# Optimization experiments

Measured on AMD Instinct MI355X. Metric: run time of the kernel, lower is better.

The kernel has to match this reference:

```python
import jax, jax.numpy as jnp
import numpy as np

H_SPLITS = [2, 3, 3]          # crpe_window {3:2, 5:3, 7:3}
K_SIZES = [3, 5, 7]
NUM_HEADS = 8
EPS = 1e-6


def dwconv(x, w, b, k):
    # x: (B,C,H,W), w: (C,1,k,k) depthwise, 'same' padding
    y = jax.lax.conv_general_dilated(
        x, w, (1, 1), [(k // 2, k // 2)] * 2,
        feature_group_count=x.shape[1],
        dimension_numbers=('NCHW', 'OIHW', 'NCHW'))
    return y + b[None, :, None, None]


def layernorm(x, g, b):
    m = jnp.mean(x, -1, keepdims=True)
    v = jnp.var(x, -1, keepdims=True)
    return (x - m) * jax.lax.rsqrt(v + EPS) * g + b


def conv_rel_pos_enc(q, v, ws, bs, H, W):
    # ConvRelPosEnc (MPViT style, no cls token): q * depthwise_conv(v)
    B, h, N, Ch = q.shape
    v_img = v.transpose(0, 1, 3, 2).reshape(B, h * Ch, H, W)  # B (h Ch) H W
    splits = np.cumsum([hs * Ch for hs in H_SPLITS])[:-1]
    parts = jnp.split(v_img, splits, axis=1)
    conv_v = jnp.concatenate(
        [dwconv(p, w, b, k) for p, w, b, k in zip(parts, ws, bs, K_SIZES)], axis=1)
    conv_v = conv_v.reshape(B, h, Ch, N).transpose(0, 1, 3, 2)
    return q * conv_v


def setup_inputs() -> dict:
    key = jax.random.key(0)
    B, H, W, C, nd, r, mr = 8, 64, 64, 320, 4, 2, 4
    h = NUM_HEADS
    N = H * W
    Ch = C // h
    hid = C // r
    ks = jax.random.split(key, 16)
    s = 0.02
    return {
        'x': jax.random.normal(ks[0], (B, N, C), jnp.float32),
        'domain_label': jax.nn.one_hot(jax.random.randint(ks[1], (B,), 0, nd), nd, dtype=jnp.float32),
        'cpe_w': jax.random.normal(ks[2], (C, 1, 3, 3), jnp.float32) * s,
        'cpe_b': jnp.zeros((C,), jnp.float32),
        'ln1_g': jnp.ones((C,), jnp.float32), 'ln1_b': jnp.zeros((C,), jnp.float32),
        'qkv_w': jax.random.normal(ks[3], (3 * C, C), jnp.float32) * s,
        'qkv_b': jnp.zeros((3 * C,), jnp.float32),
        'crpe_w3': jax.random.normal(ks[4], (2 * Ch, 1, 3, 3), jnp.float32) * s,
        'crpe_b3': jnp.zeros((2 * Ch,), jnp.float32),
        'crpe_w5': jax.random.normal(ks[5], (3 * Ch, 1, 5, 5), jnp.float32) * s,
        'crpe_b5': jnp.zeros((3 * Ch,), jnp.float32),
        'crpe_w7': jax.random.normal(ks[6], (3 * Ch, 1, 7, 7), jnp.float32) * s,
        'crpe_b7': jnp.zeros((3 * Ch,), jnp.float32),
        'dom_w1': jax.random.normal(ks[7], (hid, nd), jnp.float32) * s,
        'dom_b1': jnp.zeros((hid,), jnp.float32),
        'dom_w2': jax.random.normal(ks[8], (C, hid), jnp.float32) * s,
        'dom_b2': jnp.zeros((C,), jnp.float32),
        'proj_w': jax.random.normal(ks[9], (C, C), jnp.float32) * s,
        'proj_b': jnp.zeros((C,), jnp.float32),
        'ln2_g': jnp.ones((C,), jnp.float32), 'ln2_b': jnp.zeros((C,), jnp.float32),
        'mlp_w1': jax.random.normal(ks[10], (mr * C, C), jnp.float32) * s,
        'mlp_b1': jnp.zeros((mr * C,), jnp.float32),
        'mlp_w2': jax.random.normal(ks[11], (C, mr * C), jnp.float32) * s,
        'mlp_b2': jnp.zeros((C,), jnp.float32),
        'H': H, 'W': W,
    }


def reference(x, domain_label, cpe_w, cpe_b, ln1_g, ln1_b, qkv_w, qkv_b,
              crpe_w3, crpe_b3, crpe_w5, crpe_b5, crpe_w7, crpe_b7,
              dom_w1, dom_b1, dom_w2, dom_b2, proj_w, proj_b,
              ln2_g, ln2_b, mlp_w1, mlp_b1, mlp_w2, mlp_b2, H, W):
    B, N, C = x.shape
    h = NUM_HEADS
    Ch = C // h
    scale = Ch ** -0.5
    # ConvPosEnc: depthwise 3x3 conv + residual
    img = x.transpose(0, 2, 1).reshape(B, C, H, W)
    x = (dwconv(img, cpe_w, cpe_b, 3) + img).reshape(B, C, N).transpose(0, 2, 1)
    # FactorAtt_ConvRelPosEnc_Sup
    cur = layernorm(x, ln1_g, ln1_b)
    qkv = (cur @ qkv_w.T + qkv_b).reshape(B, N, 3, h, Ch).transpose(2, 0, 3, 1, 4)
    q, k, v = qkv[0], qkv[1], qkv[2]          # (B,h,N,Ch) each
    k_sm = jax.nn.softmax(k, axis=2)          # softmax over tokens
    kv = jnp.einsum('bhnk,bhnv->bhkv', k_sm, v)   # (B,h,Ch,Ch)
    fa = jnp.einsum('bhnk,bhkv->bhnv', q, kv)
    fa = scale * fa + conv_rel_pos_enc(
        q, v, (crpe_w3, crpe_w5, crpe_w7), (crpe_b3, crpe_b5, crpe_b7), H, W)
    # domain gate: MLP(one_hot) -> softmax over heads, broadcast over tokens
    d = jax.nn.relu(domain_label @ dom_w1.T + dom_b1) @ dom_w2.T + dom_b2  # (B,C)
    d = jax.nn.softmax(d.reshape(B, h, 1, Ch), axis=1)
    att = (d * fa).transpose(0, 2, 1, 3).reshape(B, N, C)
    x = x + (att @ proj_w.T + proj_b)
    # MLP (GELU, ratio 4)
    cur = layernorm(x, ln2_g, ln2_b)
    cur = jax.nn.gelu(cur @ mlp_w1.T + mlp_b1, approximate=False) @ mlp_w2.T + mlp_b2
    return x + cur
```

## Files before the change

kernel.cpp:

```cpp
#include <hip/hip_runtime.h>
#include <hip/hip_bf16.h>
#include <math.h>
#include <type_traits>

#define B_    8
#define Nn    4096
#define Cc    320
#define QS    1024
#define ATT_SCALE 0.15811388300841897f

typedef __attribute__((ext_vector_type(8))) short s8v;
typedef __attribute__((ext_vector_type(4))) float f4v;

__device__ __forceinline__ float bf2f(short u) {
    return __uint_as_float(((unsigned int)(unsigned short)u) << 16);
}
__device__ __forceinline__ short f2bf(float f) {
    return (short)__bfloat16_as_ushort(__float2bfloat16(f));
}
__device__ __forceinline__ float gelu_fast(float v) {
    float u = v * (0.7978845608f + 0.0356774081f * v * v);
    float e = __expf(2.f * u);
    float t = 1.f - 2.f / (e + 1.f);
    return 0.5f * v * (1.f + t);
}

typedef const __attribute__((address_space(1))) unsigned int* gp1_t;
typedef __attribute__((address_space(3))) unsigned int* lp3_t;
__device__ __forceinline__ void gload16(const void* g, void* l) {
    __builtin_amdgcn_global_load_lds((gp1_t)g, (lp3_t)l, 16, 0, 0);
}

__global__ void cvt_all(const float* __restrict__ s0, const float* __restrict__ s1,
                        const float* __restrict__ s2, const float* __restrict__ s3,
                        __hip_bfloat16* __restrict__ d) {
    int i = blockIdx.x * 256 + threadIdx.x;
    if (i >= 1351680) return;
    const float* s; int j, rows, K;
    if (i < 327680)      { s = s0; j = i;          rows = 960;  K = 320; }
    else if (i < 450560) { s = s1; j = i - 327680; rows = 320;  K = 320; }
    else if (i < 860160) { s = s2; j = i - 450560; rows = 1280; K = 320; }
    else                 { s = s3; j = i - 860160; rows = 320;  K = 1280; }
    float v = (j / K < rows) ? s[j] : 0.f;
    d[i] = __float2bfloat16(v);
}

template<typename T>
__global__ void ln_kernel(const T* __restrict__ x, const float* __restrict__ g,
                          const float* __restrict__ bt, __hip_bfloat16* __restrict__ out) {
    int bn = blockIdx.x;
    int lane = threadIdx.x;
    const T* row = x + (size_t)bn * Cc;
    float v[5];
    float s = 0.f, s2 = 0.f;
    #pragma unroll
    for (int i = 0; i < 5; ++i) {
        if constexpr (std::is_same<T, float>::value) v[i] = row[lane + 64 * i];
        else v[i] = bf2f(((const short*)row)[lane + 64 * i]);
        s += v[i];
        s2 += v[i] * v[i];
    }
    #pragma unroll
    for (int off = 32; off > 0; off >>= 1) {
        s  += __shfl_down(s, off);
        s2 += __shfl_down(s2, off);
    }
    s  = __shfl(s, 0);
    s2 = __shfl(s2, 0);
    float mean = s * (1.f / 320.f);
    float var  = s2 * (1.f / 320.f) - mean * mean;
    float rstd = rsqrtf(var + 1e-6f);
    __hip_bfloat16* orow = out + (size_t)bn * Cc;
    #pragma unroll
    for (int i = 0; i < 5; ++i) {
        int c = lane + 64 * i;
        orow[c] = __float2bfloat16((v[i] - mean) * rstd * g[c] + bt[c]);
    }
}

template<int ACT, int RES, int WF32, int WBF16, int KT>
__global__ __launch_bounds__(512) void gemm_mfma(
        const __hip_bfloat16* __restrict__ A, const __hip_bfloat16* __restrict__ W,
        const float* __restrict__ bias, const void* __restrict__ resv,
        float* __restrict__ outf, __hip_bfloat16* __restrict__ outb,
        int NS, int Nreal, int gy) {
    constexpr int NSTEP = KT / 32;
    __shared__ __align__(16) short As[2][256 * 32];
    __shared__ __align__(16) short Bs[2][128 * 32];
    int bid = blockIdx.x;
    int grp8 = gy << 3;
    int grp = bid / grp8, rem = bid % grp8;
    int m0 = ((grp << 3) + (rem & 7)) << 8;
    int n0 = (rem >> 3) << 7;
    int tid = threadIdx.x;
    int w = tid >> 6, lane = tid & 63;
    int wr = w >> 1, wc = w & 1;
    int lrow = lane & 15, lk = lane >> 4;
    f4v acc[4][4];
    #pragma unroll
    for (int i = 0; i < 4; ++i)
        #pragma unroll
        for (int j = 0; j < 4; ++j) acc[i][j] = (f4v){0.f, 0.f, 0.f, 0.f};

    int ua0 = (w << 6) + lane;
    auto STAGE = [&](int buf, int k0) {
        #pragma unroll
        for (int i = 0; i < 2; ++i) {
            int u = ua0 + i * 512;
            int row = u >> 2, slot = u & 3;
            int sk = (slot ^ (row & 3)) << 3;
            gload16(&A[(size_t)(m0 + row) * KT + k0 + sk], &As[buf][i * 4096 + w * 512]);
        }
        {
            int u = ua0;
            int row = u >> 2, slot = u & 3;
            int sk = (slot ^ (row & 3)) << 3;
            gload16(&W[(size_t)(n0 + row) * KT + k0 + sk], &Bs[buf][w * 512]);
        }
    };

    STAGE(0, 0);
    #pragma unroll
    for (int step = 0; step < NSTEP; ++step) {
        int buf = step & 1;
        if (step + 1 < NSTEP) {
            STAGE(buf ^ 1, (step + 1) * 32);
            asm volatile("s_waitcnt vmcnt(3)" ::: "memory");
        } else {
            asm volatile("s_waitcnt vmcnt(0)" ::: "memory");
        }
        __builtin_amdgcn_sched_barrier(0);
        __builtin_amdgcn_s_barrier();
        s8v af[4], bf[4];
        #pragma unroll
        for (int mi = 0; mi < 4; ++mi) {
            int row = wr * 64 + mi * 16 + lrow;
            af[mi] = *reinterpret_cast<const s8v*>(&As[buf][row * 32 + ((lk ^ (row & 3)) << 3)]);
        }
        #pragma unroll
        for (int ni = 0; ni < 4; ++ni) {
            int row = wc * 64 + ni * 16 + lrow;
            bf[ni] = *reinterpret_cast<const s8v*>(&Bs[buf][row * 32 + ((lk ^ (row & 3)) << 3)]);
        }
        #pragma unroll
        for (int mi = 0; mi < 4; ++mi)
            #pragma unroll
            for (int ni = 0; ni < 4; ++ni)
                acc[mi][ni] = __builtin_amdgcn_mfma_f32_16x16x32_bf16(bf[ni], af[mi], acc[mi][ni], 0, 0, 0);
        __builtin_amdgcn_s_barrier();
    }
    #pragma unroll
    for (int mi = 0; mi < 4; ++mi) {
        int m = m0 + wr * 64 + mi * 16 + lrow;
        #pragma unroll
        for (int ni = 0; ni < 4; ++ni) {
            int n = n0 + wc * 64 + ni * 16 + (lk << 2);
            if (n >= Nreal) continue;
            f4v v4 = acc[mi][ni];
            float4 bv = *reinterpret_cast<const float4*>(&bias[n]);
            v4[0] += bv.x; v4[1] += bv.y; v4[2] += bv.z; v4[3] += bv.w;
            if (RES == 1) {
                const float* res = (const float*)resv;
                float4 rv = *reinterpret_cast<const float4*>(&res[(size_t)m * NS + n]);
                v4[0] += rv.x; v4[1] += rv.y; v4[2] += rv.z; v4[3] += rv.w;
            } else if (RES == 2) {
                const short* res = (const short*)resv;
                short4 rv = *reinterpret_cast<const short4*>(&res[(size_t)m * NS + n]);
                v4[0] += bf2f(rv.x); v4[1] += bf2f(rv.y);
                v4[2] += bf2f(rv.z); v4[3] += bf2f(rv.w);
            }
            if (ACT == 1) {
                #pragma unroll
                for (int r = 0; r < 4; ++r) v4[r] = gelu_fast(v4[r]);
            }
            if (WF32)
                *reinterpret_cast<float4*>(&outf[(size_t)m * NS + n]) =
                    make_float4(v4[0], v4[1], v4[2], v4[3]);
            if (WBF16) {
                ushort4 u;
                u.x = (unsigned short)f2bf(v4[0]);
                u.y = (unsigned short)f2bf(v4[1]);
                u.z = (unsigned short)f2bf(v4[2]);
                u.w = (unsigned short)f2bf(v4[3]);
                *reinterpret_cast<ushort4*>(&outb[(size_t)m * NS + n]) = u;
            }
        }
    }
}

template<int ACT, int RES, int WF32, int WBF16, int KT, int LN>
__global__ __launch_bounds__(512) void gemm_fulln(
        const __hip_bfloat16* __restrict__ A, const __hip_bfloat16* __restrict__ W,
        const float* __restrict__ bias, const void* __restrict__ resv,
        float* __restrict__ outf, __hip_bfloat16* __restrict__ outb, int NS,
        const float* __restrict__ lng, const float* __restrict__ lnb,
        __hip_bfloat16* __restrict__ lnout) {
    __shared__ __align__(16) short As[64 * 64];
    __shared__ __align__(16) short Ws[320 * 64];
    int tid = threadIdx.x;
    int m0 = blockIdx.x << 6;
    int w = tid >> 6, lane = tid & 63;
    int wr = w >> 2, wc = w & 3;
    int lrow = lane & 15, lk = lane >> 4;
    f4v acc[2][5];
    #pragma unroll
    for (int i = 0; i < 2; ++i)
        #pragma unroll
        for (int j = 0; j < 5; ++j) acc[i][j] = (f4v){0.f, 0.f, 0.f, 0.f};

    int srow = tid >> 3;
    int slot = tid & 7;

    #pragma unroll
    for (int k0 = 0; k0 < KT; k0 += 64) {
        __syncthreads();
        {
            int sk = (slot ^ (srow & 7)) << 3;
            gload16(&A[(size_t)(m0 + srow) * KT + k0 + sk], &As[w * 512]);
        }
        #pragma unroll
        for (int i = 0; i < 5; ++i) {
            int row = i * 64 + srow;
            int sk = (slot ^ (row & 7)) << 3;
            gload16(&W[(size_t)row * KT + k0 + sk], &Ws[i * 4096 + w * 512]);
        }
        __syncthreads();
        #pragma unroll
        for (int ks = 0; ks < 2; ++ks) {
            s8v af[2], bf[5];
            #pragma unroll
            for (int mi = 0; mi < 2; ++mi) {
                int row = wr * 32 + mi * 16 + lrow;
                int s = (ks * 4 + lk) ^ (row & 7);
                af[mi] = *reinterpret_cast<const s8v*>(&As[row * 64 + s * 8]);
            }
            #pragma unroll
            for (int ni = 0; ni < 5; ++ni) {
                int row = wc * 80 + ni * 16 + lrow;
                int s = (ks * 4 + lk) ^ (row & 7);
                bf[ni] = *reinterpret_cast<const s8v*>(&Ws[row * 64 + s * 8]);
            }
            #pragma unroll
            for (int mi = 0; mi < 2; ++mi)
                #pragma unroll
                for (int ni = 0; ni < 5; ++ni)
                    acc[mi][ni] = __builtin_amdgcn_mfma_f32_16x16x32_bf16(bf[ni], af[mi], acc[mi][ni], 0, 0, 0);
        }
    }
    float psum[2] = {0.f, 0.f}, psq[2] = {0.f, 0.f};
    #pragma unroll
    for (int mi = 0; mi < 2; ++mi) {
        int rl = wr * 32 + mi * 16 + lrow;
        int m = m0 + rl;
        #pragma unroll
        for (int ni = 0; ni < 5; ++ni) {
            int n = wc * 80 + ni * 16 + (lk << 2);
            f4v v4 = acc[mi][ni];
            float4 bv = *reinterpret_cast<const float4*>(&bias[n]);
            v4[0] += bv.x; v4[1] += bv.y; v4[2] += bv.z; v4[3] += bv.w;
            if (RES == 1) {
                const float* res = (const float*)resv;
                float4 rv = *reinterpret_cast<const float4*>(&res[(size_t)m * NS + n]);
                v4[0] += rv.x; v4[1] += rv.y; v4[2] += rv.z; v4[3] += rv.w;
            } else if (RES == 2) {
                const short* res = (const short*)resv;
                short4 rv = *reinterpret_cast<const short4*>(&res[(size_t)m * NS + n]);
                v4[0] += bf2f(rv.x); v4[1] += bf2f(rv.y);
                v4[2] += bf2f(rv.z); v4[3] += bf2f(rv.w);
            }
            if (ACT == 1) {
                #pragma unroll
                for (int r = 0; r < 4; ++r) v4[r] = gelu_fast(v4[r]);
            }
            if (WF32)
                *reinterpret_cast<float4*>(&outf[(size_t)m * NS + n]) =
                    make_float4(v4[0], v4[1], v4[2], v4[3]);
            if (WBF16) {
                ushort4 u;
                u.x = (unsigned short)f2bf(v4[0]);
                u.y = (unsigned short)f2bf(v4[1]);
                u.z = (unsigned short)f2bf(v4[2]);
                u.w = (unsigned short)f2bf(v4[3]);
                *reinterpret_cast<ushort4*>(&outb[(size_t)m * NS + n]) = u;
            }
            if (LN) {
                acc[mi][ni] = v4;
                psum[mi] += v4[0] + v4[1] + v4[2] + v4[3];
                psq[mi]  += v4[0]*v4[0] + v4[1]*v4[1] + v4[2]*v4[2] + v4[3]*v4[3];
            }
        }
    }
    if (LN) {
        __syncthreads();
        float* red = (float*)As;
        #pragma unroll
        for (int mi = 0; mi < 2; ++mi) {
            int rl = wr * 32 + mi * 16 + lrow;
            red[(rl * 16 + wc * 4 + lk) * 2]     = psum[mi];
            red[(rl * 16 + wc * 4 + lk) * 2 + 1] = psq[mi];
        }
        __syncthreads();
        float* st = (float*)Ws;
        if (tid < 64) {
            float s = 0.f, q = 0.f;
            #pragma unroll
            for (int p = 0; p < 16; ++p) {
                s += red[(tid * 16 + p) * 2];
                q += red[(tid * 16 + p) * 2 + 1];
            }
            float mean = s * (1.f / 320.f);
            float var  = q * (1.f / 320.f) - mean * mean;
            st[tid * 2]     = mean;
            st[tid * 2 + 1] = rsqrtf(var + 1e-6f);
        }
        __syncthreads();
        #pragma unroll
        for (int mi = 0; mi < 2; ++mi) {
            int rl = wr * 32 + mi * 16 + lrow;
            int m = m0 + rl;
            float mean = st[rl * 2], rstd = st[rl * 2 + 1];
            #pragma unroll
            for (int ni = 0; ni < 5; ++ni) {
                int n = wc * 80 + ni * 16 + (lk << 2);
                float4 g4 = *reinterpret_cast<const float4*>(&lng[n]);
                float4 b4 = *reinterpret_cast<const float4*>(&lnb[n]);
                f4v v4 = acc[mi][ni];
                ushort4 u;
                u.x = (unsigned short)f2bf((v4[0] - mean) * rstd * g4.x + b4.x);
                u.y = (unsigned short)f2bf((v4[1] - mean) * rstd * g4.y + b4.y);
                u.z = (unsigned short)f2bf((v4[2] - mean) * rstd * g4.z + b4.z);
                u.w = (unsigned short)f2bf((v4[3] - mean) * rstd * g4.w + b4.w);
                *reinterpret_cast<ushort4*>(&lnout[(size_t)m * Cc + n]) = u;
            }
        }
    }
}

__global__ __launch_bounds__(256) void cpe_tile(
        const float* __restrict__ src, const float* __restrict__ wts,
        const float* __restrict__ bias, __hip_bfloat16* __restrict__ outb) {
    constexpr int P = 1, S = 18;
    __shared__ float vt[S * S * 8];
    __shared__ float ws_[8 * 9];
    int blk = blockIdx.x;
    int tile = blk & 15;
    int g  = (blk >> 4) % 40;
    int b  = (blk >> 4) / 40;
    int ty0 = (tile >> 2) << 4;
    int tx0 = (tile & 3) << 4;
    int c0 = g * 8;
    int tid = threadIdx.x;
    for (int e = tid; e < 72; e += 256) ws_[e] = wts[c0 * 9 + e];
    const float* sb = src + (size_t)b * Nn * Cc + c0;
    for (int e = tid; e < S * S; e += 256) {
        int hy = e / S, hx = e % S;
        int gy = ty0 - P + hy, gx = tx0 - P + hx;
        float px8[8];
        #pragma unroll
        for (int j = 0; j < 8; ++j) px8[j] = 0.f;
        if ((unsigned)gy < 64u && (unsigned)gx < 64u) {
            const float* p = &sb[(size_t)((gy << 6) + gx) * Cc];
            float4 lo = reinterpret_cast<const float4*>(p)[0];
            float4 hi = reinterpret_cast<const float4*>(p)[1];
            px8[0] = lo.x; px8[1] = lo.y; px8[2] = lo.z; px8[3] = lo.w;
            px8[4] = hi.x; px8[5] = hi.y; px8[6] = hi.z; px8[7] = hi.w;
        }
        #pragma unroll
        for (int j = 0; j < 8; ++j) vt[e * 8 + j] = px8[j];
    }
    __syncthreads();
    int cl  = tid & 7;
    int px  = (tid >> 3) & 15;
    int pyh = tid >> 7;
    int c = c0 + cl;
    float acc[8];
    float bval = bias[c];
    #pragma unroll
    for (int j = 0; j < 8; ++j) acc[j] = bval;
    #pragma unroll
    for (int dx = 0; dx < 3; ++dx) {
        float col[10];
        #pragma unroll
        for (int i = 0; i < 10; ++i)
            col[i] = vt[((pyh * 8 + i) * S + (px + dx)) * 8 + cl];
        #pragma unroll
        for (int j = 0; j < 8; ++j)
            #pragma unroll
            for (int dy = 0; dy < 3; ++dy)
                acc[j] += col[j + dy] * ws_[cl * 9 + dy * 3 + dx];
    }
    #pragma unroll
    for (int j = 0; j < 8; ++j) {
        int n = ((ty0 + pyh * 8 + j) << 6) + tx0 + px;
        size_t bn = (size_t)b * Nn + n;
        float ctr = vt[((pyh * 8 + j + P) * S + (px + P)) * 8 + cl];
        outb[bn * Cc + c] = __float2bfloat16(acc[j] + ctr);
    }
}

template<int KSZ>
__device__ __forceinline__ void crpe_body(
        float* vt, float* ws_, int tile, int b, int c0,
        const short* __restrict__ qkv, const float* __restrict__ wts,
        const float* __restrict__ bias,
        const short* __restrict__ fa0, const float* __restrict__ dg,
        short* __restrict__ outb) {
    constexpr int P = KSZ / 2;
    constexpr int S = 16 + 2 * P;
    int ty0 = (tile >> 2) << 4;
    int tx0 = (tile & 3) << 4;
    int tid = threadIdx.x;
    for (int e = tid; e < 8 * KSZ * KSZ; e += 256) ws_[e] = wts[e];
    const short* sb = qkv + (size_t)b * Nn * QS + 640 + c0;
    for (int e = tid; e < S * S; e += 256) {
        int hy = e / S, hx = e % S;
        int gy = ty0 - P + hy, gx = tx0 - P + hx;
        float px8[8];
        #pragma unroll
        for (int j = 0; j < 8; ++j) px8[j] = 0.f;
        if ((unsigned)gy < 64u && (unsigned)gx < 64u) {
            s8v v8 = *reinterpret_cast<const s8v*>(&sb[(size_t)((gy << 6) + gx) * QS]);
            #pragma unroll
            for (int j = 0; j < 8; ++j) px8[j] = bf2f(v8[j]);
        }
        #pragma unroll
        for (int j = 0; j < 8; ++j) vt[e * 8 + j] = px8[j];
    }
    __syncthreads();
    int cl  = tid & 7;
    int px  = (tid >> 3) & 15;
    int pyh = tid >> 7;
    int c = c0 + cl;
    float acc[8];
    float bval = bias[cl];
    #pragma unroll
    for (int j = 0; j < 8; ++j) acc[j] = bval;
    #pragma unroll
    for (int dx = 0; dx < KSZ; ++dx) {
        float col[8 + KSZ - 1];
        #pragma unroll
        for (int i = 0; i < 8 + KSZ - 1; ++i)
            col[i] = vt[((pyh * 8 + i) * S + (px + dx)) * 8 + cl];
        #pragma unroll
        for (int j = 0; j < 8; ++j)
            #pragma unroll
            for (int dy = 0; dy < KSZ; ++dy)
                acc[j] += col[j + dy] * ws_[cl * KSZ * KSZ + dy * KSZ + dx];
    }
    float dgv = dg[(size_t)b * Cc + c];
    #pragma unroll
    for (int j = 0; j < 8; ++j) {
        int n = ((ty0 + pyh * 8 + j) << 6) + tx0 + px;
        size_t bn = (size_t)b * Nn + n;
        float qv  = bf2f(qkv[bn * QS + c]);
        float fav = bf2f(fa0[bn * Cc + c]);
        float r = dgv * (ATT_SCALE * fav + qv * acc[j]);
        outb[bn * Cc + c] = __float2bfloat16(r);
    }
}

__global__ __launch_bounds__(256) void crpe_all(
        const __hip_bfloat16* __restrict__ qkv,
        const float* __restrict__ w3, const float* __restrict__ b3,
        const float* __restrict__ w5, const float* __restrict__ b5,
        const float* __restrict__ w7, const float* __restrict__ b7,
        const __hip_bfloat16* __restrict__ fa, const float* __restrict__ dg,
        __hip_bfloat16* __restrict__ outb) {
    __shared__ float vt[22 * 22 * 8];
    __shared__ float ws_[8 * 49];
    int blk = blockIdx.x;
    int tile = blk & 15;
    int g = (blk >> 4) % 40;
    int b = (blk >> 4) / 40;
    int c0 = g * 8;
    if (g < 10)
        crpe_body<3>(vt, ws_, tile, b, c0, (const short*)qkv,
                     w3 + c0 * 9, b3 + c0, (const short*)fa, dg, (short*)outb);
    else if (g < 25)
        crpe_body<5>(vt, ws_, tile, b, c0, (const short*)qkv,
                     w5 + (c0 - 80) * 25, b5 + (c0 - 80), (const short*)fa, dg, (short*)outb);
    else
        crpe_body<7>(vt, ws_, tile, b, c0, (const short*)qkv,
                     w7 + (c0 - 200) * 49, b7 + (c0 - 200), (const short*)fa, dg, (short*)outb);
}

__global__ __launch_bounds__(256) void kv_mfma(const __hip_bfloat16* __restrict__ qkv,
                                               float* __restrict__ kvp) {
    __shared__ short lds[4 * 2 * 48 * 66];
    int blk = blockIdx.x;
    int s = blk & 7;
    int bh = blk >> 3;
    int h = bh & 7, b = bh >> 3;
    int tid = threadIdx.x;
    int w = tid >> 6, lane = tid & 63;
    short* ke_t = lds + w * 2 * 48 * 66;
    short* vv_t = ke_t + 48 * 66;
    for (int e = lane; e < 8 * 66; e += 64) {
        ke_t[40 * 66 + e] = 0;
        vv_t[40 * 66 + e] = 0;
    }
    for (int n = lane; n < 66; n += 64) vv_t[40 * 66 + n] = (short)0x3F80;

    const short* kb = (const short*)qkv + (size_t)b * Nn * QS + 320 + h * 40;
    const short* vb = kb + 320;
    int col0 = lane & 15, kq = lane >> 4;
    f4v acc[3][3];
    #pragma unroll
    for (int i = 0; i < 3; ++i)
        #pragma unroll
        for (int j = 0; j < 3; ++j) acc[i][j] = (f4v){0.f, 0.f, 0.f, 0.f};

    for (int t = w; t < 8; t += 4) {
        int n0 = s * 512 + t * 64;
        for (int e = lane; e < 320; e += 64) {
            int nl = e / 5, oct = e % 5;
            size_t go = (size_t)(n0 + nl) * QS + oct * 8;
            s8v k8 = *reinterpret_cast<const s8v*>(kb + go);
            s8v v8 = *reinterpret_cast<const s8v*>(vb + go);
            #pragma unroll
            for (int j = 0; j < 8; ++j) {
                ke_t[(oct * 8 + j) * 66 + nl] = f2bf(__expf(bf2f(k8[j])));
                vv_t[(oct * 8 + j) * 66 + nl] = v8[j];
            }
        }
        __syncthreads();
        #pragma unroll
        for (int ks = 0; ks < 2; ++ks) {
            s8v af[3], bfr[3];
            #pragma unroll
            for (int mt = 0; mt < 3; ++mt)
                af[mt] = *reinterpret_cast<const s8v*>(ke_t + (mt * 16 + col0) * 66 + ks * 32 + kq * 8);
            #pragma unroll
            for (int nt = 0; nt < 3; ++nt)
                bfr[nt] = *reinterpret_cast<const s8v*>(vv_t + (nt * 16 + col0) * 66 + ks * 32 + kq * 8);
            #pragma unroll
            for (int mt = 0; mt < 3; ++mt)
                #pragma unroll
                for (int nt = 0; nt < 3; ++nt)
                    acc[mt][nt] = __builtin_amdgcn_mfma_f32_16x16x32_bf16(af[mt], bfr[nt], acc[mt][nt], 0, 0, 0);
        }
        __syncthreads();
    }
    float* red = (float*)lds;
    #pragma unroll
    for (int mt = 0; mt < 3; ++mt) {
        #pragma unroll
        for (int nt = 0; nt < 3; ++nt) {
            #pragma unroll
            for (int r = 0; r < 4; ++r) {
                int ch = mt * 16 + kq * 4 + r;
                int cv = nt * 16 + col0;
                if (ch < 40) red[w * 1920 + ch * 48 + cv] = acc[mt][nt][r];
            }
        }
    }
    __syncthreads();
    for (int p = tid; p < 1920; p += 256) {
        float sv = red[p] + red[1920 + p] + red[2 * 1920 + p] + red[3 * 1920 + p];
        kvp[(size_t)blk * 1920 + p] = sv;
    }
}

__global__ void kv_combine2(const float* __restrict__ kvp, float* __restrict__ kv) {
    int bh = blockIdx.x;
    int tid = threadIdx.x;
    __shared__ float sinv[40];
    if (tid < 40) {
        float S = 0.f;
        for (int s2 = 0; s2 < 8; ++s2)
            S += kvp[(size_t)(bh * 8 + s2) * 1920 + tid * 48 + 40];
        sinv[tid] = 1.f / S;
    }
    __syncthreads();
    for (int p = tid; p < 1600; p += 256) {
        int ch = p / 40, cv = p % 40;
        float v = 0.f;
        for (int s2 = 0; s2 < 8; ++s2)
            v += kvp[(size_t)(bh * 8 + s2) * 1920 + ch * 48 + cv];
        kv[(size_t)bh * 1600 + p] = v * sinv[ch];
    }
}

__global__ void dgate_kernel(const float* __restrict__ lbl, const float* __restrict__ w1,
                             const float* __restrict__ b1, const float* __restrict__ w2,
                             const float* __restrict__ b2, float* __restrict__ dg) {
    int b = blockIdx.x;
    int tid = threadIdx.x;
    __shared__ float hid[160];
    __shared__ float dd[320];
    if (tid < 160) {
        float a = b1[tid];
        for (int d = 0; d < 4; ++d) a += w1[tid * 4 + d] * lbl[b * 4 + d];
        hid[tid] = fmaxf(a, 0.f);
    }
    __syncthreads();
    float a = b2[tid];
    for (int j = 0; j < 160; ++j) a += w2[tid * 160 + j] * hid[j];
    dd[tid] = a;
    __syncthreads();
    if (tid < 40) {
        float M = -1e30f;
        for (int h2 = 0; h2 < 8; ++h2) M = fmaxf(M, dd[h2 * 40 + tid]);
        float S = 0.f;
        float e[8];
        for (int h2 = 0; h2 < 8; ++h2) { e[h2] = __expf(dd[h2 * 40 + tid] - M); S += e[h2]; }
        float inv = 1.f / S;
        for (int h2 = 0; h2 < 8; ++h2) dg[b * 320 + h2 * 40 + tid] = e[h2] * inv;
    }
}

__global__ __launch_bounds__(256) void fa_kernel(const __hip_bfloat16* __restrict__ qkv,
        const float* __restrict__ kvmat, __hip_bfloat16* __restrict__ fa) {
    __shared__ float kvs[1600];
    int blk = blockIdx.x;
    int chunk = blk & 15;
    int bh = blk >> 4;
    int h = bh & 7, b = bh >> 3;
    int tid = threadIdx.x;
    for (int e = tid; e < 1600; e += 256) kvs[e] = kvmat[(size_t)bh * 1600 + e];
    __syncthreads();
    int n = chunk * 256 + tid;
    const short* qr = (const short*)qkv + (size_t)(b * Nn + n) * QS + h * 40;
    float q[40];
    #pragma unroll
    for (int i = 0; i < 5; ++i) {
        s8v v8 = reinterpret_cast<const s8v*>(qr)[i];
        #pragma unroll
        for (int j = 0; j < 8; ++j) q[i * 8 + j] = bf2f(v8[j]);
    }
    float o[40];
    #pragma unroll
    for (int cv = 0; cv < 40; ++cv) o[cv] = 0.f;
    #pragma unroll
    for (int ch = 0; ch < 40; ++ch) {
        float qv = q[ch];
        #pragma unroll
        for (int cv = 0; cv < 40; ++cv)
            o[cv] += qv * kvs[ch * 40 + cv];
    }
    short* fr = (short*)fa + (size_t)(b * Nn + n) * 320 + h * 40;
    #pragma unroll
    for (int i = 0; i < 5; ++i) {
        s8v u;
        #pragma unroll
        for (int j = 0; j < 8; ++j) u[j] = f2bf(o[i * 8 + j]);
        *reinterpret_cast<s8v*>(fr + i * 8) = u;
    }
}

extern "C" void kernel_launch(void* const* d_in, const int* in_sizes, int n_in,
                              void* d_out, int out_size, void* d_ws, size_t ws_size,
                              hipStream_t stream) {
    const float* x     = (const float*)d_in[0];
    const float* lbl   = (const float*)d_in[1];
    const float* cpe_w = (const float*)d_in[2];
    const float* cpe_b = (const float*)d_in[3];
    const float* ln1g  = (const float*)d_in[4];
    const float* ln1b  = (const float*)d_in[5];
    const float* qkv_w = (const float*)d_in[6];
    const float* qkv_b = (const float*)d_in[7];
    const float* w3    = (const float*)d_in[8];
    const float* b3    = (const float*)d_in[9];
    const float* w5    = (const float*)d_in[10];
    const float* b5    = (const float*)d_in[11];
    const float* w7    = (const float*)d_in[12];
    const float* b7    = (const float*)d_in[13];
    const float* dw1   = (const float*)d_in[14];
    const float* db1   = (const float*)d_in[15];
    const float* dw2   = (const float*)d_in[16];
    const float* db2   = (const float*)d_in[17];
    const float* pw    = (const float*)d_in[18];
    const float* pb    = (const float*)d_in[19];
    const float* ln2g  = (const float*)d_in[20];
    const float* ln2b  = (const float*)d_in[21];
    const float* m1w   = (const float*)d_in[22];
    const float* m1b   = (const float*)d_in[23];
    const float* m2w   = (const float*)d_in[24];
    const float* m2b   = (const float*)d_in[25];
    float* out = (float*)d_out;

    float* ws = (float*)d_ws;
    __hip_bfloat16* x1b  = (__hip_bfloat16*)ws; ws += 5242880;
    __hip_bfloat16* qkvb = (__hip_bfloat16*)ws; ws += 16777216;
    float* big  = ws; ws += 20971520;
    __hip_bfloat16* gelub = (__hip_bfloat16*)big;
    __hip_bfloat16* fab   = (__hip_bfloat16*)ws; ws += 5242880;
    __hip_bfloat16* bb1   = (__hip_bfloat16*)ws; ws += 5242880;
    __hip_bfloat16* wb    = (__hip_bfloat16*)ws; ws += 675840;
    float* kvp  = ws; ws += 983040;
    float* kv   = ws; ws += 102400;
    float* dg   = ws; ws += 2560;
    __hip_bfloat16* wbq  = wb;
    __hip_bfloat16* wbp  = wbq  + 1024 * 320;
    __hip_bfloat16* wbm1 = wbp  + 384 * 320;
    __hip_bfloat16* wbm2 = wbm1 + 1280 * 320;

    cvt_all<<<5280, 256, 0, stream>>>(qkv_w, pw, m1w, m2w, wb);
    cpe_tile<<<B_ * 40 * 16, 256, 0, stream>>>(x, cpe_w, cpe_b, x1b);
    ln_kernel<__hip_bfloat16><<<B_ * Nn, 64, 0, stream>>>(x1b, ln1g, ln1b, bb1);
    gemm_mfma<0, 0, 0, 1, 320><<<1024, 512, 0, stream>>>(bb1, wbq, qkv_b, nullptr,
                                                         nullptr, qkvb, QS, 960, 8);
    kv_mfma<<<512, 256, 0, stream>>>(qkvb, kvp);
    kv_combine2<<<64, 256, 0, stream>>>(kvp, kv);
    dgate_kernel<<<B_, 320, 0, stream>>>(lbl, dw1, db1, dw2, db2, dg);
    fa_kernel<<<B_ * 8 * 16, 256, 0, stream>>>(qkvb, kv, fab);
    crpe_all<<<B_ * 40 * 16, 256, 0, stream>>>(qkvb, w3, b3, w5, b5, w7, b7,
                                               fab, dg, bb1);
    gemm_fulln<0, 2, 1, 0, 320, 1><<<512, 512, 0, stream>>>(bb1, wbp, pb, x1b,
                                                            out, nullptr, 320,
                                                            ln2g, ln2b, bb1);
    gemm_mfma<1, 0, 0, 1, 320><<<1280, 512, 0, stream>>>(bb1, wbm1, m1b, nullptr,
                                                         nullptr, gelub, 1280, 1280, 10);
    gemm_fulln<0, 1, 1, 0, 1280, 0><<<512, 512, 0, stream>>>(gelub, wbm2, m2b, out,
                                                             out, nullptr, 320,
                                                             nullptr, nullptr, nullptr);
}
```

Baseline: 299.2 us.

## Swap pipelining schemes between tiled GEMM and full-N fused GEMM kernels

The large tiled GEMM drops its double-buffered K=32 async prefetch and uses a single-buffered K=64 tile with block-wide syncs. The full-N GEMM with fused LayerNorm gains a double-buffered K=32 pipeline with prefetch and vmcnt waits. The aim is to balance LDS usage and overlap between the two kernels. The cost is that the main GEMM loses its load/compute overlap.

```diff
diff --git a/kernel.cpp b/kernel.cpp
--- a/kernel.cpp
+++ b/kernel.cpp
@@ -84,9 +84,8 @@
         const float* __restrict__ bias, const void* __restrict__ resv,
         float* __restrict__ outf, __hip_bfloat16* __restrict__ outb,
         int NS, int Nreal, int gy) {
-    constexpr int NSTEP = KT / 32;
-    __shared__ __align__(16) short As[2][256 * 32];
-    __shared__ __align__(16) short Bs[2][128 * 32];
+    __shared__ __align__(16) short As[256 * 64];
+    __shared__ __align__(16) short Bs[128 * 64];
     int bid = blockIdx.x;
     int grp8 = gy << 3;
     int grp = bid / grp8, rem = bid % grp8;
@@ -102,52 +101,46 @@
         #pragma unroll
         for (int j = 0; j < 4; ++j) acc[i][j] = (f4v){0.f, 0.f, 0.f, 0.f};
 
-    int ua0 = (w << 6) + lane;
-    auto STAGE = [&](int buf, int k0) {
+    int srow = (w << 3) + (lane >> 3);
+    int slot = lane & 7;
+
+    #pragma unroll
+    for (int k0 = 0; k0 < KT; k0 += 64) {
+        __syncthreads();
+        #pragma unroll
+        for (int i = 0; i < 4; ++i) {
+            int row = i * 64 + srow;
+            int sk = (slot ^ (row & 7)) << 3;
+            gload16(&A[(size_t)(m0 + row) * KT + k0 + sk], &As[i * 4096 + w * 512]);
+        }
         #pragma unroll
         for (int i = 0; i < 2; ++i) {
-            int u = ua0 + i * 512;
-            int row = u >> 2, slot = u & 3;
-            int sk = (slot ^ (row & 3)) << 3;
-            gload16(&A[(size_t)(m0 + row) * KT + k0 + sk], &As[buf][i * 4096 + w * 512]);
-        }
-        {
-            int u = ua0;
-            int row = u >> 2, slot = u & 3;
-            int sk = (slot ^ (row & 3)) << 3;
-            gload16(&W[(size_t)(n0 + row) * KT + k0 + sk], &Bs[buf][w * 512]);
-        }
-    };
-
-    STAGE(0, 0);
-    #pragma unroll
-    for (int step = 0; step < NSTEP; ++step) {
-        int buf = step & 1;
-        if (step + 1 < NSTEP) {
-            STAGE(buf ^ 1, (step + 1) * 32);
-            asm volatile("s_waitcnt vmcnt(3)" ::: "memory");
-        } else {
-            asm volatile("s_waitcnt vmcnt(0)" ::: "memory");
-        }
-        __builtin_amdgcn_sched_barrier(0);
-        __builtin_amdgcn_s_barrier();
-        s8v af[4], bf[4];
-        #pragma unroll
-        for (int mi = 0; mi < 4; ++mi) {
-            int row = wr * 64 + mi * 16 + lrow;
-            af[mi] = *reinterpret_cast<const s8v*>(&As[buf][row * 32 + ((lk ^ (row & 3)) << 3)]);
-        }
-        #pragma unroll
-        for (int ni = 0; ni < 4; ++ni) {
-            int row = wc * 64 + ni * 16 + lrow;
-            bf[ni] = *reinterpret_cast<const s8v*>(&Bs[buf][row * 32 + ((lk ^ (row & 3)) << 3)]);
-        }
-        #pragma unroll
-        for (int mi = 0; mi < 4; ++mi)
-            #pragma unroll
-            for (int ni = 0; ni < 4; ++ni)
-                acc[mi][ni] = __builtin_amdgcn_mfma_f32_16x16x32_bf16(bf[ni], af[mi], acc[mi][ni], 0, 0, 0);
-        __builtin_amdgcn_s_barrier();
+            int row = i * 64 + srow;
+            int sk = (slot ^ (row & 7)) << 3;
+            gload16(&W[(size_t)(n0 + row) * KT + k0 + sk], &Bs[i * 4096 + w * 512]);
+        }
+        __syncthreads();
+        #pragma unroll
+        for (int ks = 0; ks < 2; ++ks) {
+            s8v af[4], bf[4];
+            #pragma unroll
+            for (int mi = 0; mi < 4; ++mi) {
+                int row = wr * 64 + mi * 16 + lrow;
+                int s = (ks * 4 + lk) ^ (row & 7);
+                af[mi] = *reinterpret_cast<const s8v*>(&As[row * 64 + s * 8]);
+            }
+            #pragma unroll
+            for (int ni = 0; ni < 4; ++ni) {
+                int row = wc * 64 + ni * 16 + lrow;
+                int s = (ks * 4 + lk) ^ (row & 7);
+                bf[ni] = *reinterpret_cast<const s8v*>(&Bs[row * 64 + s * 8]);
+            }
+            #pragma unroll
+            for (int mi = 0; mi < 4; ++mi)
+                #pragma unroll
+                for (int ni = 0; ni < 4; ++ni)
+                    acc[mi][ni] = __builtin_amdgcn_mfma_f32_16x16x32_bf16(bf[ni], af[mi], acc[mi][ni], 0, 0, 0);
+        }
     }
     #pragma unroll
     for (int mi = 0; mi < 4; ++mi) {
@@ -195,8 +188,9 @@
         float* __restrict__ outf, __hip_bfloat16* __restrict__ outb, int NS,
         const float* __restrict__ lng, const float* __restrict__ lnb,
         __hip_bfloat16* __restrict__ lnout) {
-    __shared__ __align__(16) short As[64 * 64];
-    __shared__ __align__(16) short Ws[320 * 64];
+    constexpr int NSTEP = KT / 32;
+    __shared__ __align__(16) short As[2][64 * 32];
+    __shared__ __align__(16) short Ws[2][320 * 32];
     int tid = threadIdx.x;
     int m0 = blockIdx.x << 6;
     int w = tid >> 6, lane = tid & 63;
@@ -208,45 +202,56 @@
         #pragma unroll
         for (int j = 0; j < 5; ++j) acc[i][j] = (f4v){0.f, 0.f, 0.f, 0.f};
 
-    int srow = tid >> 3;
-    int slot = tid & 7;
-
-    #pragma unroll
-    for (int k0 = 0; k0 < KT; k0 += 64) {
-        __syncthreads();
-        {
-            int sk = (slot ^ (srow & 7)) << 3;
-            gload16(&A[(size_t)(m0 + srow) * KT + k0 + sk], &As[w * 512]);
-        }
-        #pragma unroll
-        for (int i = 0; i < 5; ++i) {
-            int row = i * 64 + srow;
-            int sk = (slot ^ (row & 7)) << 3;
-            gload16(&W[(size_t)row * KT + k0 + sk], &Ws[i * 4096 + w * 512]);
-        }
-        __syncthreads();
-        #pragma unroll
-        for (int ks = 0; ks < 2; ++ks) {
-            s8v af[2], bf[5];
-            #pragma unroll
-            for (int mi = 0; mi < 2; ++mi) {
-                int row = wr * 32 + mi * 16 + lrow;
-                int s = (ks * 4 + lk) ^ (row & 7);
-                af[mi] = *reinterpret_cast<const s8v*>(&As[row * 64 + s * 8]);
-            }
-            #pragma unroll
-            for (int ni = 0; ni < 5; ++ni) {
-                int row = wc * 80 + ni * 16 + lrow;
-                int s = (ks * 4 + lk) ^ (row & 7);
-                bf[ni] = *reinterpret_cast<const s8v*>(&Ws[row * 64 + s * 8]);
-            }
-            #pragma unroll
-            for (int mi = 0; mi < 2; ++mi)
-                #pragma unroll
-                for (int ni = 0; ni < 5; ++ni)
-                    acc[mi][ni] = __builtin_amdgcn_mfma_f32_16x16x32_bf16(bf[ni], af[mi], acc[mi][ni], 0, 0, 0);
-        }
-    }
+    auto STAGE = [&](int buf, int k0) {
+        #pragma unroll
+        for (int i = 0; i < 3; ++i) {
+            int u = tid + i * 512;
+            if (i == 0 && w < 4) {
+                int row = u >> 2, slot = u & 3;
+                int sk = (slot ^ (row & 3)) << 3;
+                gload16(&A[(size_t)(m0 + row) * KT + k0 + sk],
+                        &As[buf][(w << 6) * 8]);
+            } else {
+                int uw = u - 256;
+                int row = uw >> 2, slot = uw & 3;
+                int sk = (slot ^ (row & 3)) << 3;
+                gload16(&W[(size_t)row * KT + k0 + sk],
+                        &Ws[buf][((w << 6) + i * 512 - 256) * 8]);
+            }
+        }
+    };
+
+    STAGE(0, 0);
+    #pragma unroll
+    for (int step = 0; step < NSTEP; ++step) {
+        int buf = step & 1;
+        if (step + 1 < NSTEP) {
+            STAGE(buf ^ 1, (step + 1) * 32);
+            asm volatile("s_waitcnt vmcnt(3)" ::: "memory");
+        } else {
+            asm volatile("s_waitcnt vmcnt(0)" ::: "memory");
+        }
+        __builtin_amdgcn_sched_barrier(0);
+        __builtin_amdgcn_s_barrier();
+        s8v af[2], bf[5];
+        #pragma unroll
+        for (int mi = 0; mi < 2; ++mi) {
+            int row = wr * 32 + mi * 16 + lrow;
+            af[mi] = *reinterpret_cast<const s8v*>(&As[buf][row * 32 + ((lk ^ (row & 3)) << 3)]);
+        }
+        #pragma unroll
+        for (int ni = 0; ni < 5; ++ni) {
+            int row = wc * 80 + ni * 16 + lrow;
+            bf[ni] = *reinterpret_cast<const s8v*>(&Ws[buf][row * 32 + ((lk ^ (row & 3)) << 3)]);
+        }
+        #pragma unroll
+        for (int mi = 0; mi < 2; ++mi)
+            #pragma unroll
+            for (int ni = 0; ni < 5; ++ni)
+                acc[mi][ni] = __builtin_amdgcn_mfma_f32_16x16x32_bf16(bf[ni], af[mi], acc[mi][ni], 0, 0, 0);
+        __builtin_amdgcn_s_barrier();
+    }
+
     float psum[2] = {0.f, 0.f}, psq[2] = {0.f, 0.f};
     #pragma unroll
     for (int mi = 0; mi < 2; ++mi) {
```

After: 308.5 us. 3.1% more time.
